# Optimization experiments

Measured on AMD Instinct MI355X. Metric: run time of the kernel, lower is better.

## Reference

```python
import jax, jax.numpy as jnp
import numpy as np

N = 100_000      # nodes
E = 1_600_000    # edges
F_IN = 128       # node_features
H1, H2 = 50, 20  # GCLSTM hidden sizes (fixed in the model)


def _norm_weights(src, dst, w, n):
    # PyG get_laplacian(sym): remove self loops, deg over row, sym-normalize.
    w = jnp.where(src == dst, jnp.zeros_like(w), w)  # remove self-loops (weight 0)
    deg = jax.ops.segment_sum(w, src, num_segments=n)
    deg_safe = jnp.where(deg > 0, deg, jnp.ones_like(deg))
    dis = jnp.where(deg > 0, deg_safe ** -0.5, jnp.zeros_like(deg))
    return dis[src] * w * dis[dst]


def _lhat_matvec(x, src, dst, wn, n):
    # L_hat = 2*L/lambda_max - I with sym norm and lambda_max=2  =>  -D^-1/2 A D^-1/2
    return -jax.ops.segment_sum(wn[:, None] * x[src], dst, num_segments=n)


def _gclstm_cell(x, src, dst, wn, n, Wx, bx, theta, bconv, out_ch):
    # One GCLSTM step with H = C = 0 (the model passes H=C=None).
    H = jnp.zeros((n, out_ch), x.dtype)
    C = jnp.zeros((n, out_ch), x.dtype)
    # ChebConv(H) for all 4 gates: Tx_0 = H, Tx_1 = L_hat @ H   (K = 2)
    Tx = jnp.stack([H, _lhat_matvec(H, src, dst, wn, n)])       # [2, n, out]
    conv = jnp.einsum('knf,gkfo->gno', Tx, theta) + bconv[:, None, :]  # [4, n, out]
    Z = x @ Wx + bx                                              # [n, 4*out], gates i,f,c,o
    zi, zf, zc, zo = jnp.split(Z, 4, axis=-1)
    I = jax.nn.sigmoid(zi + conv[0])
    Fg = jax.nn.sigmoid(zf + conv[1])
    T = jnp.tanh(zc + conv[2])
    C = Fg * C + I * T
    O = jax.nn.sigmoid(zo + conv[3])
    return O * jnp.tanh(C)


def setup_inputs() -> dict:
    key = jax.random.key(0)
    ks = jax.random.split(key, 14)
    s = 0.1  # param init scale
    return {
        'x': jax.random.normal(ks[0], (N, F_IN), jnp.float32),
        'edge_index': jax.random.randint(ks[1], (2, E), 0, N, dtype=jnp.int32),
        'edge_weight': jax.random.uniform(ks[2], (E,), jnp.float32),
        # layer 1: W_x for gates i,f,c,o concatenated, Cheb thetas [gate, K, in, out]
        'Wx1': s * jax.random.normal(ks[3], (F_IN, 4 * H1), jnp.float32),
        'bx1': s * jax.random.normal(ks[4], (4 * H1,), jnp.float32),
        'theta1': s * jax.random.normal(ks[5], (4, 2, H1, H1), jnp.float32),
        'bconv1': s * jax.random.normal(ks[6], (4, H1), jnp.float32),
        # layer 2
        'Wx2': s * jax.random.normal(ks[7], (H1, 4 * H2), jnp.float32),
        'bx2': s * jax.random.normal(ks[8], (4 * H2,), jnp.float32),
        'theta2': s * jax.random.normal(ks[9], (4, 2, H2, H2), jnp.float32),
        'bconv2': s * jax.random.normal(ks[10], (4, H2), jnp.float32),
        # linear head
        'Wl': s * jax.random.normal(ks[11], (H2, 1), jnp.float32),
        'bl': s * jax.random.normal(ks[12], (1,), jnp.float32),
    }


def reference(x, edge_index, edge_weight, Wx1, bx1, theta1, bconv1,
              Wx2, bx2, theta2, bconv2, Wl, bl):
    src, dst = edge_index[0], edge_index[1]
    wn = _norm_weights(src, dst, edge_weight, N)
    h = _gclstm_cell(x, src, dst, wn, N, Wx1, bx1, theta1, bconv1, H1)
    h = _gclstm_cell(h, src, dst, wn, N, Wx2, bx2, theta2, bconv2, H2)
    h = jax.nn.relu(h)
    # F.dropout: identity at inference (deterministic baseline)
    return h @ Wl + bl  # [N, 1]
```

## Files before the change

### kernel.cpp

```cpp
#include <hip/hip_runtime.h>
#include <hip/hip_bf16.h>


#define NODES 100000
#define NTILES 6250

typedef float v4f   __attribute__((ext_vector_type(4)));
typedef float fragC __attribute__((ext_vector_type(4)));
typedef short frag8 __attribute__((ext_vector_type(8)));

#define OFF_B1H 0
#define OFF_B2H 40960
#define OFF_PB1 49152
#define OFF_PB2 49792

__device__ __forceinline__ unsigned short f2bf(float f) {
  unsigned int u = __float_as_uint(f);
  u += 0x7fffu + ((u >> 16) & 1u);
  return (unsigned short)(u >> 16);
}
__device__ __forceinline__ float fsig(float z) {
  float t = __builtin_amdgcn_exp2f(z * -1.44269504088896f);
  return __builtin_amdgcn_rcpf(1.0f + t);
}
__device__ __forceinline__ float ftanh(float z) {
  float t = __builtin_amdgcn_exp2f(z * 2.88539008177793f);
  return 1.0f - 2.0f * __builtin_amdgcn_rcpf(t + 1.0f);
}

union bfu { __hip_bfloat162 h; unsigned int u; };

__device__ __forceinline__ void cvt8(const float* v, frag8& hi, frag8& lo) {
  float lof[8];
#pragma unroll
  for (int p = 0; p < 4; ++p) {
    bfu c; c.h = __float22bfloat162_rn(make_float2(v[2 * p], v[2 * p + 1]));
    hi[2 * p]     = (short)(c.u & 0xffffu);
    hi[2 * p + 1] = (short)(c.u >> 16);
    lof[2 * p]     = v[2 * p]     - __uint_as_float((c.u & 0xffffu) << 16);
    lof[2 * p + 1] = v[2 * p + 1] - __uint_as_float(c.u & 0xffff0000u);
  }
#pragma unroll
  for (int p = 0; p < 4; ++p) {
    bfu c; c.h = __float22bfloat162_rn(make_float2(lof[2 * p], lof[2 * p + 1]));
    lo[2 * p]     = (short)(c.u & 0xffffu);
    lo[2 * p + 1] = (short)(c.u >> 16);
  }
}

__global__ void pack_weights(const float* __restrict__ Wx1, const float* __restrict__ bx1,
                             const float* __restrict__ bconv1,
                             const float* __restrict__ Wx2, const float* __restrict__ bx2,
                             const float* __restrict__ bconv2,
                             unsigned char* __restrict__ ws) {
  const int tid = blockIdx.x * blockDim.x + threadIdx.x;
  const int stride = gridDim.x * blockDim.x;
  unsigned short* B1H = (unsigned short*)(ws + OFF_B1H);
  unsigned short* B2H = (unsigned short*)(ws + OFF_B2H);
  float* PB1 = (float*)(ws + OFF_PB1);
  float* PB2 = (float*)(ws + OFF_PB2);

  for (int idx = tid; idx < 20480; idx += stride) {
    int j = idx & 7, lane = (idx >> 3) & 63, ft = idx >> 9;
    int s = ft / 10, t = ft % 10;
    int k = 32 * s + ((lane >> 4) << 3) + j;
    int m = lane & 15;
    int c = -1, g = 0;
    if (t <= 8) { g = t % 3; c = 16 * (t / 3) + m; }
    else if (m < 6) { c = 48 + m / 3; g = m % 3; }
    float val = 0.f;
    if (c >= 0) {
      int gs = (g == 0) ? 0 : (g == 1) ? 2 : 3;
      val = Wx1[k * 200 + gs * 50 + c];
    }
    B1H[idx] = f2bf(val);
  }
  for (int idx = tid; idx < 4096; idx += stride) {
    int j = idx & 7, lane = (idx >> 3) & 63, ft = idx >> 9;
    int s = ft >> 2, t = ft & 3;
    int k = 32 * s + ((lane >> 4) << 3) + j;
    int m = lane & 15;
    int c = -1, g = 0;
    if (t <= 2) { g = t; c = m; }
    else if (m < 12) { c = 16 + m / 3; g = m % 3; }
    float val = 0.f;
    if (c >= 0 && k < 50) {
      int gs = (g == 0) ? 0 : (g == 1) ? 2 : 3;
      val = Wx2[k * 80 + gs * 20 + c];
    }
    B2H[idx] = f2bf(val);
  }
  for (int idx = tid; idx < 160; idx += stride) {
    int t = idx >> 4, m = idx & 15;
    int c = -1, g = 0;
    if (t <= 8) { g = t % 3; c = 16 * (t / 3) + m; }
    else if (m < 6) { c = 48 + m / 3; g = m % 3; }
    float v = 0.f;
    if (c >= 0) {
      int gs = (g == 0) ? 0 : (g == 1) ? 2 : 3;
      v = bx1[gs * 50 + c] + bconv1[gs * 50 + c];
    }
    PB1[idx] = v;
  }
  for (int idx = tid; idx < 64; idx += stride) {
    int t = idx >> 4, m = idx & 15;
    int c = -1, g = 0;
    if (t <= 2) { g = t; c = m; }
    else if (m < 12) { c = 16 + m / 3; g = m % 3; }
    float v = 0.f;
    if (c >= 0) {
      int gs = (g == 0) ? 0 : (g == 1) ? 2 : 3;
      v = bx2[gs * 20 + c] + bconv2[gs * 20 + c];
    }
    PB2[idx] = v;
  }
}

__global__ __launch_bounds__(256, 3) void gclstm_main(
    const float* __restrict__ x, const unsigned char* __restrict__ wsb,
    const float* __restrict__ Wl, const float* __restrict__ bl,
    float* __restrict__ out) {
  __shared__ unsigned short sH[4][16 * 72];

  const int tid = threadIdx.x;
  const int lane = tid & 63;
  const int wave = tid >> 6;
  const int m = lane & 15;
  const int q = lane >> 4;
  const int tau = blockIdx.x * 4 + wave;
  if (tau >= NTILES) return;

  unsigned short* sHw = (unsigned short*)sH + wave * (16 * 72);

  {
    int r0 = lane >> 2, c0 = 48 + (lane & 3) * 4;
    *(unsigned long long*)(sHw + r0 * 72 + c0) = 0ull;
  }

  const float* pb1 = (const float*)(wsb + OFF_PB1);
  const float* pb2 = (const float*)(wsb + OFF_PB2);
  float bias1v[10], bias2v[4];
#pragma unroll
  for (int t = 0; t < 10; ++t) bias1v[t] = pb1[16 * t + m];
#pragma unroll
  for (int t = 0; t < 4; ++t) bias2v[t] = pb2[16 * t + m];

  const float* xr = x + (size_t)(tau * 16 + m) * 128 + q * 8;
  v4f xb[8];
#pragma unroll
  for (int s = 0; s < 4; ++s) {
    xb[2 * s] = *(const v4f*)(xr + 32 * s);
    xb[2 * s + 1] = *(const v4f*)(xr + 32 * s + 4);
  }

  const frag8* g1 = (const frag8*)(wsb + OFF_B1H);
  fragC acc[10];
#pragma unroll
  for (int t = 0; t < 10; ++t)
    acc[t] = (fragC){bias1v[t], bias1v[t], bias1v[t], bias1v[t]};
#pragma unroll
  for (int s = 0; s < 4; ++s) {
    float av[8];
    *(v4f*)av = xb[2 * s];
    *(v4f*)(av + 4) = xb[2 * s + 1];
    frag8 ah, al;
    cvt8(av, ah, al);
#pragma unroll
    for (int t = 0; t < 10; ++t) {
      frag8 b = g1[(s * 10 + t) * 64 + lane];
      acc[t] = __builtin_amdgcn_mfma_f32_16x16x32_bf16(ah, b, acc[t], 0, 0, 0);
      acc[t] = __builtin_amdgcn_mfma_f32_16x16x32_bf16(al, b, acc[t], 0, 0, 0);
    }
    __builtin_amdgcn_sched_barrier(0);
  }

#pragma unroll
  for (int b = 0; b < 3; ++b)
#pragma unroll
    for (int r = 0; r < 4; ++r) {
      float I = fsig(acc[3 * b][r]);
      float T = ftanh(acc[3 * b + 1][r]);
      float O = fsig(acc[3 * b + 2][r]);
      sHw[(q * 4 + r) * 72 + 16 * b + m] = f2bf(O * ftanh(I * T));
    }
#pragma unroll
  for (int r = 0; r < 4; ++r) {
    float vI = __shfl(acc[9][r], 16 * q + m);
    float vT = __shfl(acc[9][r], 16 * q + m + 1);
    float vO = __shfl(acc[9][r], 16 * q + m + 2);
    if (m == 0 || m == 3) {
      float I = fsig(vI), T = ftanh(vT), O = fsig(vO);
      sHw[(q * 4 + r) * 72 + 48 + (m >> 1)] = f2bf(O * ftanh(I * T));
    }
  }

  const frag8* g2 = (const frag8*)(wsb + OFF_B2H);
  frag8 hh[2];
#pragma unroll
  for (int s = 0; s < 2; ++s)
    hh[s] = *(const frag8*)(sHw + m * 72 + 32 * s + 8 * q);
  fragC acc2[4];
#pragma unroll
  for (int t = 0; t < 4; ++t)
    acc2[t] = (fragC){bias2v[t], bias2v[t], bias2v[t], bias2v[t]};
#pragma unroll
  for (int s = 0; s < 2; ++s)
#pragma unroll
    for (int t = 0; t < 4; ++t) {
      frag8 b = g2[(s * 4 + t) * 64 + lane];
      acc2[t] = __builtin_amdgcn_mfma_f32_16x16x32_bf16(hh[s], b, acc2[t], 0, 0, 0);
    }

  const float wlm = Wl[m];
  const float wlx = (m < 4) ? Wl[16 + m] : 0.f;
  const float blv = bl[0];
  v4f res;
#pragma unroll
  for (int r = 0; r < 4; ++r) {
    float I = fsig(acc2[0][r]);
    float T = ftanh(acc2[1][r]);
    float O = fsig(acc2[2][r]);
    float h2 = O * ftanh(I * T);
    float part = fmaxf(h2, 0.f) * wlm;
    float eI = __shfl(acc2[3][r], 16 * q + 3 * m);
    float eT = __shfl(acc2[3][r], 16 * q + 3 * m + 1);
    float eO = __shfl(acc2[3][r], 16 * q + 3 * m + 2);
    float I2 = fsig(eI), T2 = ftanh(eT), O2 = fsig(eO);
    float h2x = O2 * ftanh(I2 * T2);
    part += fmaxf(h2x, 0.f) * wlx;
    part += __shfl_xor(part, 1);
    part += __shfl_xor(part, 2);
    part += __shfl_xor(part, 4);
    part += __shfl_xor(part, 8);
    res[r] = part + blv;
  }
  if (m == 0) *(v4f*)(out + tau * 16 + 4 * q) = res;
}

extern "C" void kernel_launch(void* const* d_in, const int* in_sizes, int n_in,
                              void* d_out, int out_size, void* d_ws, size_t ws_size,
                              hipStream_t stream) {
  (void)in_sizes; (void)n_in; (void)out_size; (void)ws_size;
  const float* x = (const float*)d_in[0];
  const float* Wx1 = (const float*)d_in[3];
  const float* bx1 = (const float*)d_in[4];
  const float* bconv1 = (const float*)d_in[6];
  const float* Wx2 = (const float*)d_in[7];
  const float* bx2 = (const float*)d_in[8];
  const float* bconv2 = (const float*)d_in[10];
  const float* Wl = (const float*)d_in[11];
  const float* bl = (const float*)d_in[12];
  unsigned char* ws = (unsigned char*)d_ws;

  hipLaunchKernelGGL(pack_weights, dim3(32), dim3(256), 0, stream,
                     Wx1, bx1, bconv1, Wx2, bx2, bconv2, ws);
  hipLaunchKernelGGL(gclstm_main, dim3((NTILES + 3) / 4), dim3(256), 0, stream,
                     x, ws, Wl, bl, (float*)d_out);
}
```

Before: 132.5 us.

## Drop bf16 low-part MFMA and double-buffer layer-1 weight fragment loads

```diff
diff --git a/kernel.cpp b/kernel.cpp
--- a/kernel.cpp
+++ b/kernel.cpp
@@ -30,22 +30,15 @@
 
 union bfu { __hip_bfloat162 h; unsigned int u; };
 
-__device__ __forceinline__ void cvt8(const float* v, frag8& hi, frag8& lo) {
-  float lof[8];
+__device__ __forceinline__ frag8 cvt8hi(const float* v) {
+  frag8 hi;
 #pragma unroll
   for (int p = 0; p < 4; ++p) {
     bfu c; c.h = __float22bfloat162_rn(make_float2(v[2 * p], v[2 * p + 1]));
     hi[2 * p]     = (short)(c.u & 0xffffu);
     hi[2 * p + 1] = (short)(c.u >> 16);
-    lof[2 * p]     = v[2 * p]     - __uint_as_float((c.u & 0xffffu) << 16);
-    lof[2 * p + 1] = v[2 * p + 1] - __uint_as_float(c.u & 0xffff0000u);
-  }
-#pragma unroll
-  for (int p = 0; p < 4; ++p) {
-    bfu c; c.h = __float22bfloat162_rn(make_float2(lof[2 * p], lof[2 * p + 1]));
-    lo[2 * p]     = (short)(c.u & 0xffffu);
-    lo[2 * p + 1] = (short)(c.u >> 16);
-  }
+  }
+  return hi;
 }
 
 __global__ void pack_weights(const float* __restrict__ Wx1, const float* __restrict__ bx1,
@@ -116,7 +109,7 @@
   }
 }
 
-__global__ __launch_bounds__(256, 3) void gclstm_main(
+__global__ __launch_bounds__(256, 2) void gclstm_main(
     const float* __restrict__ x, const unsigned char* __restrict__ wsb,
     const float* __restrict__ Wl, const float* __restrict__ bl,
     float* __restrict__ out) {
@@ -137,6 +130,14 @@
     *(unsigned long long*)(sHw + r0 * 72 + c0) = 0ull;
   }
 
+  const float* xr = x + (size_t)(tau * 16 + m) * 128 + q * 8;
+  v4f xb[8];
+#pragma unroll
+  for (int s = 0; s < 4; ++s) {
+    xb[2 * s] = *(const v4f*)(xr + 32 * s);
+    xb[2 * s + 1] = *(const v4f*)(xr + 32 * s + 4);
+  }
+
   const float* pb1 = (const float*)(wsb + OFF_PB1);
   const float* pb2 = (const float*)(wsb + OFF_PB2);
   float bias1v[10], bias2v[4];
@@ -145,34 +146,43 @@
 #pragma unroll
   for (int t = 0; t < 4; ++t) bias2v[t] = pb2[16 * t + m];
 
-  const float* xr = x + (size_t)(tau * 16 + m) * 128 + q * 8;
-  v4f xb[8];
-#pragma unroll
-  for (int s = 0; s < 4; ++s) {
-    xb[2 * s] = *(const v4f*)(xr + 32 * s);
-    xb[2 * s + 1] = *(const v4f*)(xr + 32 * s + 4);
-  }
-
   const frag8* g1 = (const frag8*)(wsb + OFF_B1H);
-  fragC acc[10];
-#pragma unroll
-  for (int t = 0; t < 10; ++t)
-    acc[t] = (fragC){bias1v[t], bias1v[t], bias1v[t], bias1v[t]};
+  const frag8* g2 = (const frag8*)(wsb + OFF_B2H);
+
+  frag8 ba[10], bb[10];
+#pragma unroll
+  for (int t = 0; t < 10; ++t) ba[t] = g1[t * 64 + lane];
+
+  frag8 ah[4];
 #pragma unroll
   for (int s = 0; s < 4; ++s) {
     float av[8];
     *(v4f*)av = xb[2 * s];
     *(v4f*)(av + 4) = xb[2 * s + 1];
-    frag8 ah, al;
-    cvt8(av, ah, al);
-#pragma unroll
-    for (int t = 0; t < 10; ++t) {
-      frag8 b = g1[(s * 10 + t) * 64 + lane];
-      acc[t] = __builtin_amdgcn_mfma_f32_16x16x32_bf16(ah, b, acc[t], 0, 0, 0);
-      acc[t] = __builtin_amdgcn_mfma_f32_16x16x32_bf16(al, b, acc[t], 0, 0, 0);
-    }
+    ah[s] = cvt8hi(av);
+  }
+
+  fragC acc[10];
+#pragma unroll
+  for (int t = 0; t < 10; ++t)
+    acc[t] = (fragC){bias1v[t], bias1v[t], bias1v[t], bias1v[t]};
+#pragma unroll
+  for (int s = 0; s < 4; ++s) {
+    frag8* bc = (s & 1) ? bb : ba;
+    frag8* bn = (s & 1) ? ba : bb;
+    if (s < 3) {
+#pragma unroll
+      for (int t = 0; t < 10; ++t) bn[t] = g1[((s + 1) * 10 + t) * 64 + lane];
+    }
+#pragma unroll
+    for (int t = 0; t < 10; ++t)
+      acc[t] = __builtin_amdgcn_mfma_f32_16x16x32_bf16(ah[s], bc[t], acc[t], 0, 0, 0);
     __builtin_amdgcn_sched_barrier(0);
   }
+
+  frag8 b2f[8];
+#pragma unroll
+  for (int i = 0; i < 8; ++i) b2f[i] = g2[i * 64 + lane];
 
 #pragma unroll
   for (int b = 0; b < 3; ++b)
@@ -194,7 +204,6 @@
     }
   }
 
-  const frag8* g2 = (const frag8*)(wsb + OFF_B2H);
   frag8 hh[2];
 #pragma unroll
   for (int s = 0; s < 2; ++s)
@@ -206,10 +215,8 @@
 #pragma unroll
   for (int s = 0; s < 2; ++s)
 #pragma unroll
-    for (int t = 0; t < 4; ++t) {
-      frag8 b = g2[(s * 4 + t) * 64 + lane];
-      acc2[t] = __builtin_amdgcn_mfma_f32_16x16x32_bf16(hh[s], b, acc2[t], 0, 0, 0);
-    }
+    for (int t = 0; t < 4; ++t)
+      acc2[t] = __builtin_amdgcn_mfma_f32_16x16x32_bf16(hh[s], b2f[s * 4 + t], acc2[t], 0, 0, 0);
 
   const float wlm = Wl[m];
   const float wlx = (m < 4) ? Wl[16 + m] : 0.f;
```

Result: faster. 129.7 us (-2.1%).
